# Optimization experiments

Hardware: AMD Instinct MI355X
Metric: run time of the kernel (lower is better)

The kernel has to match this reference:

```python
import jax, jax.numpy as jnp
import numpy as np

B, N, D = 8, 2048, 1024
NEG = -1e9


def setup_inputs() -> dict:
    key = jax.random.key(0)
    kx, kl, kq, kk, kv, ko = jax.random.split(key, 6)
    x = jax.random.normal(kx, (B, N, D), dtype=jnp.float32)
    # prefix padding mask: each clip has a random valid length in [N//2, N]
    lengths = jax.random.randint(kl, (B,), N // 2, N + 1)
    mask = jnp.arange(N)[None, :] < lengths[:, None]  # [B, N] bool
    s = 1.0 / np.sqrt(D)
    Wq = jax.random.normal(kq, (D, D), dtype=jnp.float32) * s  # nn.Linear weight [out,in]
    Wk = jax.random.normal(kk, (D, D), dtype=jnp.float32) * s
    Wv = jax.random.normal(kv, (D, D), dtype=jnp.float32) * s
    Wo = jax.random.normal(ko, (D, D), dtype=jnp.float32) * s
    return {"x": x, "mask": mask, "Wq": Wq, "Wk": Wk, "Wv": Wv, "Wo": Wo}


def reference(x, mask, Wq, Wk, Wv, Wo):
    # Linear (no bias): y = x @ W.T
    K = jnp.einsum('bnd,ed->bne', x, Wk)
    Q = jnp.einsum('bnd,ed->bne', x, Wq) * 0.06
    V = jnp.einsum('bnd,ed->bne', x, Wv)
    logits = jnp.einsum('bne,bme->bnm', Q, K)  # [B, N, N]
    # attention_mask = outer product of padding mask (matmul of mask with its transpose)
    attn_mask = mask[:, :, None] & mask[:, None, :]
    logits = jnp.where(attn_mask, logits, NEG)
    att_weights = jax.nn.softmax(logits, axis=-1)
    # dropout (p=0.5) is identity in eval mode
    # y = (V^T @ W)^T  ->  y[b,i,:] = sum_j att[b,j,i] * V[b,j,:]
    y = jnp.einsum('bji,bjd->bid', att_weights, V)
    y = jnp.einsum('bid,ed->bie', y, Wo)
    return (y, att_weights)
```

## Files before the change

### kernel.cpp

```cpp
#include <hip/hip_runtime.h>
#include <math.h>

typedef __attribute__((ext_vector_type(8))) short short8;
typedef __attribute__((ext_vector_type(4))) float f32x4;

namespace {
constexpr int B_ = 8;
constexpr int N_ = 2048;
constexpr int D_ = 1024;
constexpr float NEGV = -1.0e9f;
}

__device__ __forceinline__ unsigned short f2bf(float x) {
    union { float f; unsigned u; } v; v.f = x;
    unsigned u = v.u + 0x7fffu + ((v.u >> 16) & 1u);
    return (unsigned short)(u >> 16);
}

__global__ __launch_bounds__(256)
void k_lengths(const unsigned char* __restrict__ mask, int* __restrict__ L)
{
    const int b = blockIdx.x;
    const int t = threadIdx.x;
    const bool u8 = (mask[1] != 0);
    int cnt = 0;
    if (u8) {
        for (int n = t; n < N_; n += 256)
            cnt += (mask[(size_t)b * N_ + n] != 0) ? 1 : 0;
    } else {
        const int* mi = (const int*)mask;
        for (int n = t; n < N_; n += 256)
            cnt += (mi[(size_t)b * N_ + n] != 0) ? 1 : 0;
    }
    __shared__ int red[256];
    red[t] = cnt;
    __syncthreads();
    for (int s = 128; s > 0; s >>= 1) {
        if (t < s) red[t] += red[t + s];
        __syncthreads();
    }
    if (t == 0) L[b] = red[0];
}

__global__ __launch_bounds__(256)
void convert_bf16(const float* __restrict__ in, unsigned short* __restrict__ out,
                  int n4, float alpha)
{
    const int i = blockIdx.x * 256 + threadIdx.x;
    if (i >= n4) return;
    const float4 v = ((const float4*)in)[i];
    ushort4 o;
    o.x = f2bf(v.x * alpha); o.y = f2bf(v.y * alpha);
    o.z = f2bf(v.z * alpha); o.w = f2bf(v.w * alpha);
    ((ushort4*)out)[i] = o;
}

template <int OUT_MODE>
__global__ __launch_bounds__(256)
void gemm_nt_mfma(const unsigned short* __restrict__ A, int lda, long strideA,
                  const unsigned short* __restrict__ Bm, int ldb, long strideB,
                  void* __restrict__ Cout, int ldc, long strideC,
                  int K, const int* __restrict__ Lp)
{
    __shared__ __attribute__((aligned(16))) short As[128 * 32];
    __shared__ __attribute__((aligned(16))) short Bs[128 * 32];

    const int tid  = threadIdx.x;
    const int lane = tid & 63;
    const int wave = tid >> 6;
    const int b    = blockIdx.z;
    const int m0   = blockIdx.y * 128;
    const int n0   = blockIdx.x * 128;

    const unsigned short* Ab = A  + (long)b * strideA;
    const unsigned short* Bb = Bm + (long)b * strideB;

    const int rowL = tid >> 2;
    const int rowH = (tid + 256) >> 2;
    const int seg  = (((tid & 3) ^ ((tid >> 3) & 3)) * 8);

    const unsigned short* gA0 = Ab + (long)(m0 + rowL) * lda + seg;
    const unsigned short* gA1 = Ab + (long)(m0 + rowH) * lda + seg;
    const unsigned short* gB0 = Bb + (long)(n0 + rowL) * ldb + seg;
    const unsigned short* gB1 = Bb + (long)(n0 + rowH) * ldb + seg;

    short* lA0 = As + ((tid & ~63) + 0)   * 8;
    short* lA1 = As + ((tid & ~63) + 256) * 8;
    short* lB0 = Bs + ((tid & ~63) + 0)   * 8;
    short* lB1 = Bs + ((tid & ~63) + 256) * 8;

    const int q = lane >> 4, r = lane & 15;
    const int wm = (wave & 1) * 64, wn = (wave >> 1) * 64;
    const int sphys = (q ^ ((r >> 1) & 3)) * 8;

    const short* pa[4];
    const short* pb[4];
#pragma unroll
    for (int t = 0; t < 4; ++t) {
        pa[t] = As + (wm + t * 16 + r) * 32 + sphys;
        pb[t] = Bs + (wn + t * 16 + r) * 32 + sphys;
    }

    f32x4 acc[4][4] = {};

    for (int k0 = 0; k0 < K; k0 += 32) {
        __syncthreads();
        __builtin_amdgcn_global_load_lds(
            (const __attribute__((address_space(1))) void*)(gA0 + k0),
            (__attribute__((address_space(3))) void*)lA0, 16, 0, 0);
        __builtin_amdgcn_global_load_lds(
            (const __attribute__((address_space(1))) void*)(gB0 + k0),
            (__attribute__((address_space(3))) void*)lB0, 16, 0, 0);
        __builtin_amdgcn_global_load_lds(
            (const __attribute__((address_space(1))) void*)(gA1 + k0),
            (__attribute__((address_space(3))) void*)lA1, 16, 0, 0);
        __builtin_amdgcn_global_load_lds(
            (const __attribute__((address_space(1))) void*)(gB1 + k0),
            (__attribute__((address_space(3))) void*)lB1, 16, 0, 0);
        __syncthreads();

        short8 af[4], bf[4];
#pragma unroll
        for (int t = 0; t < 4; ++t) {
            af[t] = *(const short8*)pa[t];
            bf[t] = *(const short8*)pb[t];
        }
#pragma unroll
        for (int mt = 0; mt < 4; ++mt)
#pragma unroll
            for (int nt = 0; nt < 4; ++nt)
                acc[mt][nt] = __builtin_amdgcn_mfma_f32_16x16x32_bf16(
                    af[mt], bf[nt], acc[mt][nt], 0, 0, 0);
    }

    if (OUT_MODE == 1) {
        unsigned short* C = (unsigned short*)Cout + (long)b * strideC;
#pragma unroll
        for (int mt = 0; mt < 4; ++mt)
#pragma unroll
            for (int nt = 0; nt < 4; ++nt)
#pragma unroll
                for (int rr = 0; rr < 4; ++rr) {
                    const int grow = m0 + wm + mt * 16 + q * 4 + rr;
                    const int gcol = n0 + wn + nt * 16 + r;
                    C[(long)grow * ldc + gcol] = f2bf(acc[mt][nt][rr]);
                }
    } else if (OUT_MODE == 0) {
        float* C = (float*)Cout + (long)b * strideC;
#pragma unroll
        for (int mt = 0; mt < 4; ++mt)
#pragma unroll
            for (int nt = 0; nt < 4; ++nt)
#pragma unroll
                for (int rr = 0; rr < 4; ++rr) {
                    const int grow = m0 + wm + mt * 16 + q * 4 + rr;
                    const int gcol = n0 + wn + nt * 16 + r;
                    C[(long)grow * ldc + gcol] = acc[mt][nt][rr];
                }
    } else {
        const int Lb = Lp[b];
        float* C = (float*)Cout + (long)b * strideC;
#pragma unroll
        for (int mt = 0; mt < 4; ++mt)
#pragma unroll
            for (int nt = 0; nt < 4; ++nt)
#pragma unroll
                for (int rr = 0; rr < 4; ++rr) {
                    const int grow = m0 + wm + mt * 16 + q * 4 + rr;
                    const int gcol = n0 + wn + nt * 16 + r;
                    const float val = (grow < Lb && gcol < Lb) ? acc[mt][nt][rr] : NEGV;
                    C[(long)grow * ldc + gcol] = val;
                }
    }
}

__global__ __launch_bounds__(256)
void softmax_rows(float* __restrict__ Att)
{
    const size_t row = blockIdx.x;
    float* p = Att + row * (size_t)N_;
    const int t = threadIdx.x;

    float4 v0 = *(float4*)(p + t * 4);
    float4 v1 = *(float4*)(p + 1024 + t * 4);

    float mx = fmaxf(fmaxf(fmaxf(v0.x, v0.y), fmaxf(v0.z, v0.w)),
                     fmaxf(fmaxf(v1.x, v1.y), fmaxf(v1.z, v1.w)));
#pragma unroll
    for (int o = 32; o > 0; o >>= 1) mx = fmaxf(mx, __shfl_xor(mx, o, 64));

    __shared__ float red[8];
    const int wv = t >> 6;
    if ((t & 63) == 0) red[wv] = mx;
    __syncthreads();
    mx = fmaxf(fmaxf(red[0], red[1]), fmaxf(red[2], red[3]));

    float e[8];
    e[0] = expf(v0.x - mx); e[1] = expf(v0.y - mx);
    e[2] = expf(v0.z - mx); e[3] = expf(v0.w - mx);
    e[4] = expf(v1.x - mx); e[5] = expf(v1.y - mx);
    e[6] = expf(v1.z - mx); e[7] = expf(v1.w - mx);
    float s = ((e[0] + e[1]) + (e[2] + e[3])) + ((e[4] + e[5]) + (e[6] + e[7]));
#pragma unroll
    for (int o = 32; o > 0; o >>= 1) s += __shfl_xor(s, o, 64);
    if ((t & 63) == 0) red[4 + wv] = s;
    __syncthreads();
    const float inv = 1.0f / (red[4] + red[5] + red[6] + red[7]);

    *(float4*)(p + t * 4)        = make_float4(e[0] * inv, e[1] * inv, e[2] * inv, e[3] * inv);
    *(float4*)(p + 1024 + t * 4) = make_float4(e[4] * inv, e[5] * inv, e[6] * inv, e[7] * inv);
}

__global__ __launch_bounds__(256)
void transpose_att_bf16(const float* __restrict__ att, unsigned short* __restrict__ attT)
{
    __shared__ float tile[64][65];
    const int b  = blockIdx.z;
    const int j0 = blockIdx.y * 64;
    const int i0 = blockIdx.x * 64;
    const float* src = att + (long)b * N_ * N_;
    unsigned short* dst = attT + (long)b * N_ * N_;
    const int t = threadIdx.x;
#pragma unroll
    for (int l = 0; l < 4; ++l) {
        const int idx = t + l * 256;
        const int jj = idx >> 4;
        const int i4 = (idx & 15) * 4;
        const float4 v = *(const float4*)(src + (long)(j0 + jj) * N_ + i0 + i4);
        tile[i4 + 0][jj] = v.x;
        tile[i4 + 1][jj] = v.y;
        tile[i4 + 2][jj] = v.z;
        tile[i4 + 3][jj] = v.w;
    }
    __syncthreads();
#pragma unroll
    for (int l = 0; l < 4; ++l) {
        const int idx = t + l * 256;
        const int ii = idx >> 4;
        const int j4 = (idx & 15) * 4;
        ushort4 o;
        o.x = f2bf(tile[ii][j4 + 0]);
        o.y = f2bf(tile[ii][j4 + 1]);
        o.z = f2bf(tile[ii][j4 + 2]);
        o.w = f2bf(tile[ii][j4 + 3]);
        *(ushort4*)(dst + (long)(i0 + ii) * N_ + j0 + j4) = o;
    }
}

extern "C" void kernel_launch(void* const* d_in, const int* in_sizes, int n_in,
                              void* d_out, int out_size, void* d_ws, size_t ws_size,
                              hipStream_t stream)
{
    const float* x  = (const float*)d_in[0];
    const unsigned char* mask = (const unsigned char*)d_in[1];
    const float* Wq = (const float*)d_in[2];
    const float* Wk = (const float*)d_in[3];
    const float* Wv = (const float*)d_in[4];
    const float* Wo = (const float*)d_in[5];

    float* y   = (float*)d_out;
    float* att = (float*)d_out + (size_t)B_ * N_ * D_;

    char* ws = (char*)d_ws;
    int* L = (int*)ws;
    unsigned short* Wqb = (unsigned short*)(ws + 256);
    unsigned short* Wkb = Wqb + 1048576;
    unsigned short* Wvb = Wkb + 1048576;
    unsigned short* Wob = Wvb + 1048576;
    unsigned short* xb  = Wob + 1048576;
    unsigned short* Qb  = xb + 16777216;
    unsigned short* Kb  = Qb + 16777216;
    unsigned short* VT  = Kb + 16777216;
    unsigned short* attT = Qb;
    unsigned short* ctx  = xb;

    const dim3 blk(256);
    const long ND = (long)N_ * D_;
    const long NN = (long)N_ * N_;

    k_lengths<<<dim3(B_), blk, 0, stream>>>(mask, L);

    convert_bf16<<<dim3(16384), blk, 0, stream>>>(x,  xb,  4194304, 1.0f);
    convert_bf16<<<dim3(1024),  blk, 0, stream>>>(Wq, Wqb, 262144, 0.06f);
    convert_bf16<<<dim3(1024),  blk, 0, stream>>>(Wk, Wkb, 262144, 1.0f);
    convert_bf16<<<dim3(1024),  blk, 0, stream>>>(Wv, Wvb, 262144, 1.0f);
    convert_bf16<<<dim3(1024),  blk, 0, stream>>>(Wo, Wob, 262144, 1.0f);

    gemm_nt_mfma<1><<<dim3(8, 128, 1), blk, 0, stream>>>(
        xb, D_, 0, Wqb, D_, 0, Qb, D_, 0, D_, nullptr);
    gemm_nt_mfma<1><<<dim3(8, 128, 1), blk, 0, stream>>>(
        xb, D_, 0, Wkb, D_, 0, Kb, D_, 0, D_, nullptr);

    gemm_nt_mfma<2><<<dim3(16, 16, B_), blk, 0, stream>>>(
        Qb, D_, ND, Kb, D_, ND, att, N_, NN, D_, L);

    softmax_rows<<<dim3(B_ * N_), blk, 0, stream>>>(att);

    transpose_att_bf16<<<dim3(32, 32, B_), blk, 0, stream>>>(att, attT);

    gemm_nt_mfma<1><<<dim3(128, 8, 1), blk, 0, stream>>>(
        Wvb, D_, 0, xb, D_, 0, VT, B_ * N_, 0, D_, nullptr);

    gemm_nt_mfma<1><<<dim3(8, 16, B_), blk, 0, stream>>>(
        attT, N_, NN, VT, B_ * N_, N_, ctx, D_, ND, N_, nullptr);

    gemm_nt_mfma<0><<<dim3(8, 128, 1), blk, 0, stream>>>(
        ctx, D_, 0, Wob, D_, 0, y, D_, 0, D_, nullptr);
}
```

Baseline: 764.1 us.

## Fuse Q/K/V projections into one GEMM and add XCD-aware block remapping

```diff
diff --git a/kernel.cpp b/kernel.cpp
--- a/kernel.cpp
+++ b/kernel.cpp
@@ -68,9 +68,22 @@
     const int tid  = threadIdx.x;
     const int lane = tid & 63;
     const int wave = tid >> 6;
-    const int b    = blockIdx.z;
-    const int m0   = blockIdx.y * 128;
-    const int n0   = blockIdx.x * 128;
+
+    const unsigned gx   = gridDim.x;
+    const unsigned gxy  = gx * gridDim.y;
+    const unsigned total = gxy * gridDim.z;
+    const unsigned orig = blockIdx.x + gx * blockIdx.y + gxy * blockIdx.z;
+    unsigned wg = orig;
+    if ((total & 7u) == 0u)
+        wg = (orig & 7u) * (total >> 3) + (orig >> 3);
+    const unsigned bz  = wg / gxy;
+    const unsigned rem = wg - bz * gxy;
+    const unsigned byy = rem / gx;
+    const unsigned bxx = rem - byy * gx;
+
+    const int b    = (int)bz;
+    const int m0   = (int)byy * 128;
+    const int n0   = (int)bxx * 128;
 
     const unsigned short* Ab = A  + (long)b * strideA;
     const unsigned short* Bb = Bm + (long)b * strideB;
@@ -247,6 +260,39 @@
     }
 }
 
+__global__ __launch_bounds__(256)
+void transpose_v_bf16(const unsigned short* __restrict__ qkv, unsigned short* __restrict__ vt)
+{
+    __shared__ unsigned short tile[64][68];
+    const int j0 = blockIdx.x * 64;
+    const int d0 = blockIdx.y * 64;
+    const int t = threadIdx.x;
+#pragma unroll
+    for (int l = 0; l < 4; ++l) {
+        const int idx = t + l * 256;
+        const int jj = idx >> 4;
+        const int d4 = (idx & 15) * 4;
+        const ushort4 v = *(const ushort4*)(qkv + (long)(j0 + jj) * 3072 + 2048 + d0 + d4);
+        tile[d4 + 0][jj] = v.x;
+        tile[d4 + 1][jj] = v.y;
+        tile[d4 + 2][jj] = v.z;
+        tile[d4 + 3][jj] = v.w;
+    }
+    __syncthreads();
+#pragma unroll
+    for (int l = 0; l < 4; ++l) {
+        const int idx = t + l * 256;
+        const int dd = idx >> 4;
+        const int j4 = (idx & 15) * 4;
+        ushort4 o;
+        o.x = tile[dd][j4 + 0];
+        o.y = tile[dd][j4 + 1];
+        o.z = tile[dd][j4 + 2];
+        o.w = tile[dd][j4 + 3];
+        *(ushort4*)(vt + (long)(d0 + dd) * 16384 + j0 + j4) = o;
+    }
+}
+
 extern "C" void kernel_launch(void* const* d_in, const int* in_sizes, int n_in,
                               void* d_out, int out_size, void* d_ws, size_t ws_size,
                               hipStream_t stream)
@@ -263,43 +309,38 @@
 
     char* ws = (char*)d_ws;
     int* L = (int*)ws;
-    unsigned short* Wqb = (unsigned short*)(ws + 256);
-    unsigned short* Wkb = Wqb + 1048576;
-    unsigned short* Wvb = Wkb + 1048576;
-    unsigned short* Wob = Wvb + 1048576;
-    unsigned short* xb  = Wob + 1048576;
-    unsigned short* Qb  = xb + 16777216;
-    unsigned short* Kb  = Qb + 16777216;
-    unsigned short* VT  = Kb + 16777216;
-    unsigned short* attT = Qb;
-    unsigned short* ctx  = xb;
+    unsigned short* Wqkvb = (unsigned short*)(ws + 256);
+    unsigned short* Wob   = Wqkvb + 3145728;
+    unsigned short* xb    = Wob + 1048576;
+    unsigned short* QKVb  = xb + 16777216;
+    unsigned short* VT    = QKVb + 50331648;
+    unsigned short* attT  = QKVb;
+    unsigned short* ctx   = xb;
 
     const dim3 blk(256);
+    const long NN = (long)N_ * N_;
     const long ND = (long)N_ * D_;
-    const long NN = (long)N_ * N_;
+    const long NQ = (long)N_ * 3072;
 
     k_lengths<<<dim3(B_), blk, 0, stream>>>(mask, L);
 
     convert_bf16<<<dim3(16384), blk, 0, stream>>>(x,  xb,  4194304, 1.0f);
-    convert_bf16<<<dim3(1024),  blk, 0, stream>>>(Wq, Wqb, 262144, 0.06f);
-    convert_bf16<<<dim3(1024),  blk, 0, stream>>>(Wk, Wkb, 262144, 1.0f);
-    convert_bf16<<<dim3(1024),  blk, 0, stream>>>(Wv, Wvb, 262144, 1.0f);
-    convert_bf16<<<dim3(1024),  blk, 0, stream>>>(Wo, Wob, 262144, 1.0f);
-
-    gemm_nt_mfma<1><<<dim3(8, 128, 1), blk, 0, stream>>>(
-        xb, D_, 0, Wqb, D_, 0, Qb, D_, 0, D_, nullptr);
-    gemm_nt_mfma<1><<<dim3(8, 128, 1), blk, 0, stream>>>(
-        xb, D_, 0, Wkb, D_, 0, Kb, D_, 0, D_, nullptr);
+    convert_bf16<<<dim3(1024),  blk, 0, stream>>>(Wq, Wqkvb,           262144, 0.06f);
+    convert_bf16<<<dim3(1024),  blk, 0, stream>>>(Wk, Wqkvb + 1048576, 262144, 1.0f);
+    convert_bf16<<<dim3(1024),  blk, 0, stream>>>(Wv, Wqkvb + 2097152, 262144, 1.0f);
+    convert_bf16<<<dim3(1024),  blk, 0, stream>>>(Wo, Wob,             262144, 1.0f);
+
+    gemm_nt_mfma<1><<<dim3(24, 128, 1), blk, 0, stream>>>(
+        xb, D_, 0, Wqkvb, D_, 0, QKVb, 3072, 0, D_, nullptr);
+
+    transpose_v_bf16<<<dim3(256, 16), blk, 0, stream>>>(QKVb, VT);
 
     gemm_nt_mfma<2><<<dim3(16, 16, B_), blk, 0, stream>>>(
-        Qb, D_, ND, Kb, D_, ND, att, N_, NN, D_, L);
+        QKVb, 3072, NQ, QKVb + 1024, 3072, NQ, att, N_, NN, D_, L);
 
     softmax_rows<<<dim3(B_ * N_), blk, 0, stream>>>(att);
 
     transpose_att_bf16<<<dim3(32, 32, B_), blk, 0, stream>>>(att, attT);
-
-    gemm_nt_mfma<1><<<dim3(128, 8, 1), blk, 0, stream>>>(
-        Wvb, D_, 0, xb, D_, 0, VT, B_ * N_, 0, D_, nullptr);
 
     gemm_nt_mfma<1><<<dim3(8, 16, B_), blk, 0, stream>>>(
         attT, N_, NN, VT, B_ * N_, N_, ctx, D_, ND, N_, nullptr);
```

After: 730.5 us. 1.05x faster.
